# Kernel optimization log

Hardware: AMD Instinct MI355X
Metric: run time of the kernel (lower is better)

The kernel has to match this reference:

```python
import jax, jax.numpy as jnp
import numpy as np

NUM_HEADS = 10
NEG_BIG = -2.0**32 + 1.0  # padding value used before softmax in the original
MASK_ADDER = -10000.0     # additive directional mask value


def setup_inputs() -> dict:
    key = jax.random.key(0)
    k1, k2, k3, k4, k5 = jax.random.split(key, 5)
    B, T, D, U = 8, 1024, 640, 640
    x = jax.random.normal(k1, (B, T, D), dtype=jnp.float32)
    mask = jax.random.randint(k2, (B, T), 0, 2, dtype=jnp.int32)
    s = 1.0 / np.sqrt(D)
    Wq = jax.random.normal(k3, (D, U), dtype=jnp.float32) * s
    Wk = jax.random.normal(k4, (D, U), dtype=jnp.float32) * s
    Wv = jax.random.normal(k5, (D, U), dtype=jnp.float32) * s
    return {"x": x, "mask": mask, "Wq": Wq, "Wk": Wk, "Wv": Wv}


def reference(x, mask, Wq, Wk, Wv):
    B, T, _ = x.shape
    H = NUM_HEADS
    U = Wq.shape[1]
    d = U // H

    # projections (no bias)
    Q = x @ Wq  # [B,T,U]
    K = x @ Wk
    V = x @ Wv

    # tf split(axis=2)+concat(axis=0) == head-major layout [H,B,T,d]
    def to_heads(t):
        return t.reshape(B, T, H, d).transpose(2, 0, 1, 3)

    Qh, Kh, Vh = to_heads(Q), to_heads(K), to_heads(V)

    scores = jnp.einsum('hbqd,hbkd->hbqk', Qh, Kh) / jnp.sqrt(jnp.float32(d))

    # key padding mask: sign(sum|K|) per key position
    key_m = jnp.sign(jnp.sum(jnp.abs(Kh), axis=-1))  # [H,B,T]
    scores = jnp.where(key_m[:, :, None, :] == 0, jnp.float32(NEG_BIG), scores)

    # directional mask: 'forward' -> attend strictly to past (row > col)
    row = jnp.arange(T)[:, None]
    col = jnp.arange(T)[None, :]
    allowed = (row > col).astype(scores.dtype)  # [T,T]
    scores = scores + (1.0 - allowed) * MASK_ADDER

    attn = jax.nn.softmax(scores, axis=-1)

    # post-softmax multiplicative query mask
    query_m = jnp.sign(jnp.sum(jnp.abs(Qh), axis=-1))  # [H,B,T]
    attn = attn * query_m[:, :, :, None]

    out = jnp.einsum('hbqk,hbkd->hbqd', attn, Vh)  # [H,B,T,d]
    out = out.transpose(1, 2, 0, 3).reshape(B, T, U)  # concat heads back on feature dim

    out = out * mask[:, :, None].astype(jnp.float32)
    return out
```

## Files before the change

### kernel.cpp

```cpp
#include <hip/hip_runtime.h>
#include <hip/hip_bf16.h>
#include <stdint.h>

#define B_DIM 8
#define T_DIM 1024
#define D_DIM 640
#define H_DIM 10
#define LOG2E 1.442695041f

typedef unsigned short ushort_t;
typedef __attribute__((ext_vector_type(8))) short short8;
typedef __attribute__((ext_vector_type(4))) float f32x4;
typedef __attribute__((ext_vector_type(16))) float f32x16;
typedef __attribute__((ext_vector_type(4))) unsigned int u32x4;

__device__ __forceinline__ ushort_t f32_to_bf16(float f) {
    unsigned int u = __builtin_bit_cast(unsigned int, f);
    u += 0x7fffu + ((u >> 16) & 1u);
    return (ushort_t)(u >> 16);
}
__device__ __forceinline__ float v_exp2(float x) {
    float r; asm("v_exp_f32 %0, %1" : "=v"(r) : "v"(x)); return r;
}
__device__ __forceinline__ unsigned cvt_pk_bf16(float a, float b) {
    unsigned r; asm("v_cvt_pk_bf16_f32 %0, %1, %2" : "=v"(r) : "v"(a), "v"(b)); return r;
}
__device__ __forceinline__ void gload16(const void* g, void* l) {
    auto gp = reinterpret_cast<const __attribute__((address_space(1))) uint32_t*>(
        reinterpret_cast<uintptr_t>(g));
    auto lp = reinterpret_cast<__attribute__((address_space(3))) uint32_t*>(
        reinterpret_cast<uintptr_t>(l));
    __builtin_amdgcn_global_load_lds(gp, lp, 16, 0, 0);
}

__constant__ int SPERM[32] = {0,31,30,29,28,27,26,25,24,23,22,21,20,19,18,17,
                              16,15,14,13,12,11,10,9,8,7,6,5,4,3,2,1};

__global__ __launch_bounds__(256) void convwt(
    const float* __restrict__ x,
    const float* __restrict__ Wq, const float* __restrict__ Wk, const float* __restrict__ Wv,
    ushort_t* __restrict__ xb, ushort_t* __restrict__ Wt)
{
    const int tid = threadIdx.x;
    if (blockIdx.x < 300) {
        const int w = blockIdx.x / 100, rem = blockIdx.x % 100;
        const int k0 = (rem % 10) * 64, n0 = (rem / 10) * 64;
        const float* W = (w == 0) ? Wq : (w == 1) ? Wk : Wv;
        ushort_t* Wo = Wt + (size_t)w * D_DIM * D_DIM;

        __shared__ alignas(16) ushort_t st[64][72];
        const int r = tid >> 2, cs = (tid & 3) * 16;
        #pragma unroll
        for (int j = 0; j < 4; ++j) {
            float4 v = *reinterpret_cast<const float4*>(
                &W[(size_t)(k0 + r) * D_DIM + n0 + cs + j * 4]);
            st[r][cs + j * 4 + 0] = f32_to_bf16(v.x);
            st[r][cs + j * 4 + 1] = f32_to_bf16(v.y);
            st[r][cs + j * 4 + 2] = f32_to_bf16(v.z);
            st[r][cs + j * 4 + 3] = f32_to_bf16(v.w);
        }
        __syncthreads();
        const int nr = tid >> 2, ks = (tid & 3) * 16;
        ushort_t tmp[16];
        #pragma unroll
        for (int j = 0; j < 16; ++j) tmp[j] = st[ks + j][nr];
        ushort_t* dst = &Wo[(size_t)(n0 + nr) * D_DIM + k0 + ks];
        *reinterpret_cast<short8*>(dst)     = *reinterpret_cast<const short8*>(&tmp[0]);
        *reinterpret_cast<short8*>(dst + 8) = *reinterpret_cast<const short8*>(&tmp[8]);
    } else {
        const int n8 = (B_DIM * T_DIM * D_DIM) / 8;
        for (int i = (blockIdx.x - 300) * 256 + tid; i < n8; i += 2048 * 256) {
            float4 a = *reinterpret_cast<const float4*>(&x[i * 8]);
            float4 b = *reinterpret_cast<const float4*>(&x[i * 8 + 4]);
            ushort_t o[8] = {f32_to_bf16(a.x), f32_to_bf16(a.y), f32_to_bf16(a.z), f32_to_bf16(a.w),
                             f32_to_bf16(b.x), f32_to_bf16(b.y), f32_to_bf16(b.z), f32_to_bf16(b.w)};
            *reinterpret_cast<short8*>(&xb[i * 8]) = *reinterpret_cast<const short8*>(o);
        }
    }
}

__global__ __launch_bounds__(256) void gemm_qkv(
    const ushort_t* __restrict__ xb, const ushort_t* __restrict__ Wt,
    const int* __restrict__ msk,
    ushort_t* __restrict__ QF, ushort_t* __restrict__ KF, ushort_t* __restrict__ VF,
    float* __restrict__ qs, ushort_t* __restrict__ km16)
{
    const int L = blockIdx.x;
    const int xcd = L & 7, j = L >> 3;
    const int m0 = (xcd * 8 + (j & 7)) * 128;
    const int nz = j >> 3;
    const int n0 = (nz % 5) * 128;
    const int w  = nz / 5;

    const ushort_t* Wm = Wt + (size_t)w * D_DIM * D_DIM;

    __shared__ alignas(16) ushort_t As[128 * 64];
    __shared__ alignas(16) ushort_t Bs[128 * 64];

    const int tid = threadIdx.x;
    const int lane = tid & 63, wave = tid >> 6;
    const int lo = lane & 15, g = lane >> 4;
    const int wm = wave >> 1, wn = wave & 1;
    const int srow = tid >> 3, schunk = tid & 7;

    f32x4 acc[4][4];
    #pragma unroll
    for (int i = 0; i < 4; ++i)
        #pragma unroll
        for (int jj = 0; jj < 4; ++jj) acc[i][jj] = (f32x4){0.f, 0.f, 0.f, 0.f};

    for (int k0 = 0; k0 < D_DIM; k0 += 64) {
        #pragma unroll
        for (int i = 0; i < 4; ++i) {
            int row = i * 32 + srow;
            int sc = schunk ^ (row & 7);
            gload16(&xb[(size_t)(m0 + row) * D_DIM + k0 + sc * 8], &As[i * 2048 + tid * 8]);
            gload16(&Wm[(size_t)(n0 + row) * D_DIM + k0 + sc * 8], &Bs[i * 2048 + tid * 8]);
        }
        __syncthreads();
        #pragma unroll
        for (int ks = 0; ks < 2; ++ks) {
            short8 af[4], bf[4];
            #pragma unroll
            for (int t = 0; t < 4; ++t) {
                int arow = wm * 64 + t * 16 + lo;
                int ach = (ks * 4 + g) ^ (arow & 7);
                af[t] = *reinterpret_cast<const short8*>(&As[arow * 64 + ach * 8]);
                int brow = wn * 64 + t * 16 + lo;
                int bch = (ks * 4 + g) ^ (brow & 7);
                bf[t] = *reinterpret_cast<const short8*>(&Bs[brow * 64 + bch * 8]);
            }
            __builtin_amdgcn_s_setprio(1);
            #pragma unroll
            for (int mi = 0; mi < 4; ++mi)
                #pragma unroll
                for (int ni = 0; ni < 4; ++ni)
                    acc[mi][ni] = __builtin_amdgcn_mfma_f32_16x16x32_bf16(
                        af[mi], bf[ni], acc[mi][ni], 0, 0, 0);
            __builtin_amdgcn_s_setprio(0);
        }
        __syncthreads();
    }

    const int hh = (n0 >> 6) + wn;
    const int bb = m0 >> 10;
    const int hb = hh * 8 + bb;
    const int ktw = ((m0 & 1023) >> 6) + wm;

    if (w == 2) {
        const int hiv = g >> 1, jj0 = (g & 1) * 4;
        #pragma unroll
        for (int mi = 0; mi < 4; ++mi)
            #pragma unroll
            for (int ni = 0; ni < 4; ++ni) {
                const int df = ni >> 1, l31v = (ni & 1) * 16 + lo;
                size_t idx = ((((size_t)(hb * 16 + ktw) * 4 + mi) * 2 + df) * 64
                              + hiv * 32 + l31v) * 8 + jj0;
                ushort4 o = make_ushort4(f32_to_bf16(acc[mi][ni][0]), f32_to_bf16(acc[mi][ni][1]),
                                         f32_to_bf16(acc[mi][ni][2]), f32_to_bf16(acc[mi][ni][3]));
                *reinterpret_cast<ushort4*>(&VF[idx]) = o;
            }
    } else {
        #pragma unroll
        for (int mi = 0; mi < 4; ++mi)
            #pragma unroll
            for (int r = 0; r < 4; ++r) {
                float s_ = fabsf(acc[mi][0][r]) + fabsf(acc[mi][1][r])
                         + fabsf(acc[mi][2][r]) + fabsf(acc[mi][3][r]);
                #pragma unroll
                for (int m = 1; m < 16; m <<= 1) s_ += __shfl_xor(s_, m);
                if (lo == 0) {
                    int row = m0 + wm * 64 + mi * 16 + g * 4 + r;
                    int rowid = hh * 8192 + row;
                    if (w == 0) qs[rowid] = (s_ > 0.f ? 1.f : 0.f) * (float)msk[row];
                    else        km16[rowid] = (s_ > 0.f) ? (ushort_t)0x3F80 : (ushort_t)0;
                }
            }
        const int hi2 = lo >> 3, jjq = lo & 7;
        const int s32base = ((m0 & 1023) + wm * 64) >> 5;
        #pragma unroll
        for (int mi = 0; mi < 4; ++mi)
            #pragma unroll
            for (int ni = 0; ni < 4; ++ni)
                #pragma unroll
                for (int r = 0; r < 4; ++r) {
                    int l31 = (mi & 1) * 16 + g * 4 + r;
                    if (w == 0) {
                        int s32 = s32base + (mi >> 1);
                        size_t idx = (((size_t)(hb * 32 + s32) * 4 + ni) * 64
                                      + hi2 * 32 + l31) * 8 + jjq;
                        QF[idx] = f32_to_bf16(acc[mi][ni][r]);
                    } else {
                        int f = (mi >> 1) & 1;
                        size_t idx = ((((size_t)(hb * 16 + ktw) * 2 + f) * 4 + ni) * 64
                                      + hi2 * 32 + l31) * 8 + jjq;
                        KF[idx] = f32_to_bf16(acc[mi][ni][r]);
                    }
                }
    }
}

#define LOADK(KB_, KT_IDX) do {                                                  \
    const ushort_t* KT_ = &KFh[(KT_IDX) * 4096];                                 \
    _Pragma("unroll")                                                            \
    for (int f_ = 0; f_ < 2; ++f_)                                               \
        _Pragma("unroll")                                                        \
        for (int kc_ = 0; kc_ < 4; ++kc_)                                        \
            KB_[f_][kc_] = *reinterpret_cast<const short8*>(                     \
                &KT_[(f_ * 4 + kc_) * 512 + lane * 8]);                          \
} while (0)

#define COMPUTE_TILE(KBUF, KT_IDX) do {                                          \
    const int k0_ = (KT_IDX) * 64;                                               \
    const ushort_t* VT_ = &VFh[(size_t)(KT_IDX) * 4096];                         \
    short8 vfA_[2][2], vfB_[2][2];                                               \
    _Pragma("unroll")                                                            \
    for (int c_ = 0; c_ < 2; ++c_)                                               \
        _Pragma("unroll")                                                        \
        for (int df_ = 0; df_ < 2; ++df_)                                        \
            vfA_[c_][df_] = *reinterpret_cast<const short8*>(                    \
                &VT_[(c_ * 2 + df_) * 512 + lane * 8]);                          \
    ushort4 kq_[2][4];                                                           \
    _Pragma("unroll")                                                            \
    for (int f_ = 0; f_ < 2; ++f_)                                               \
        _Pragma("unroll")                                                        \
        for (int rr_ = 0; rr_ < 4; ++rr_)                                        \
            kq_[f_][rr_] = *reinterpret_cast<const ushort4*>(                    \
                &kmr[k0_ + f_ * 32 + rr_ * 8 + hi * 4]);                         \
    unsigned pk_[2][8];                                                          \
    _Pragma("unroll")                                                            \
    for (int f_ = 0; f_ < 2; ++f_) {                                             \
        f32x16 sf_;                                                              \
        _Pragma("unroll")                                                        \
        for (int i_ = 0; i_ < 16; ++i_) sf_[i_] = 0.f;                           \
        __builtin_amdgcn_s_setprio(1);                                           \
        _Pragma("unroll")                                                        \
        for (int kc_ = 0; kc_ < 4; ++kc_)                                        \
            sf_ = __builtin_amdgcn_mfma_f32_32x32x16_bf16(KBUF[f_][kc_],         \
                                                          qf[kc_], sf_, 0, 0, 0);\
        __builtin_amdgcn_s_setprio(0);                                           \
        if (f_ == 0) {                                                           \
            _Pragma("unroll")                                                    \
            for (int c_ = 0; c_ < 2; ++c_)                                       \
                _Pragma("unroll")                                                \
                for (int df_ = 0; df_ < 2; ++df_)                                \
                    vfB_[c_][df_] = *reinterpret_cast<const short8*>(            \
                        &VT_[((c_ + 2) * 2 + df_) * 512 + lane * 8]);            \
        }                                                                        \
        _Pragma("unroll")                                                        \
        for (int rr_ = 0; rr_ < 4; ++rr_) {                                      \
            const int kbase_ = k0_ + f_ * 32 + rr_ * 8 + hi * 4;                 \
            const ushort_t* kmv_ =                                               \
                reinterpret_cast<const ushort_t*>(&kq_[f_][rr_]);                \
            float p_[4];                                                         \
            _Pragma("unroll")                                                    \
            for (int ri_ = 0; ri_ < 4; ++ri_) {                                  \
                float cc_ = (kbase_ + ri_ >= trow) ? cB : cA;                    \
                cc_ = kmv_[ri_] ? cc_ : -1e30f;                                  \
                p_[ri_] = v_exp2(fmaf(sf_[rr_ * 4 + ri_], S2, cc_));             \
                lacc += p_[ri_];                                                 \
            }                                                                    \
            pk_[f_][rr_ * 2 + 0] = cvt_pk_bf16(p_[0], p_[1]);                    \
            pk_[f_][rr_ * 2 + 1] = cvt_pk_bf16(p_[2], p_[3]);                    \
        }                                                                        \
    }                                                                            \
    _Pragma("unroll")                                                            \
    for (int c_ = 0; c_ < 4; ++c_) {                                             \
        const int f_ = c_ >> 1, o_ = (c_ & 1) * 4;                               \
        unsigned a0_ = pk_[f_][o_ + 0], b0_ = pk_[f_][o_ + 2];                   \
        unsigned a1_ = pk_[f_][o_ + 1], b1_ = pk_[f_][o_ + 3];                   \
        if (v1) {                                                                \
            asm volatile("v_permlane32_swap_b32 %0, %1" : "+v"(b0_), "+v"(a0_)); \
            asm volatile("v_permlane32_swap_b32 %0, %1" : "+v"(b1_), "+v"(a1_)); \
        } else {                                                                 \
            asm volatile("v_permlane32_swap_b32 %0, %1" : "+v"(a0_), "+v"(b0_)); \
            asm volatile("v_permlane32_swap_b32 %0, %1" : "+v"(a1_), "+v"(b1_)); \
        }                                                                        \
        u32x4 pau_ = {a0_, a1_, b0_, b1_};                                       \
        short8 pa_ = __builtin_bit_cast(short8, pau_);                           \
        short8 v0_ = (c_ < 2) ? vfA_[c_][0] : vfB_[c_ - 2][0];                   \
        short8 v1f_ = (c_ < 2) ? vfA_[c_][1] : vfB_[c_ - 2][1];                  \
        __builtin_amdgcn_s_setprio(1);                                           \
        of0 = __builtin_amdgcn_mfma_f32_32x32x16_bf16(pa_, v0_, of0, 0, 0, 0);   \
        of1 = __builtin_amdgcn_mfma_f32_32x32x16_bf16(pa_, v1f_, of1, 0, 0, 0);  \
        __builtin_amdgcn_s_setprio(0);                                           \
    }                                                                            \
} while (0)

__global__ __launch_bounds__(256, 2) void attn_wave(
    const ushort_t* __restrict__ QF, const ushort_t* __restrict__ KF,
    const ushort_t* __restrict__ VF, const float* __restrict__ qs,
    const ushort_t* __restrict__ km16, float* __restrict__ out)
{
    __shared__ float scs[4][32];
    const int tid = threadIdx.x, lane = tid & 63, wave = tid >> 6;
    const int l31 = lane & 31, hi = lane >> 5;

    const int bid = blockIdx.x, xcd = bid & 7, j = bid >> 3;
    const int g8 = xcd + 8 * (j % 10), qg = j / 10;
    const int s = SPERM[qg * 4 + wave], q0 = s * 32;
    const int b = g8 & 7, h = g8 >> 3, hb = h * 8 + b;

    unsigned pva = (unsigned)lane, pvb = 64u + (unsigned)lane;
    asm volatile("v_permlane32_swap_b32 %0, %1" : "+v"(pva), "+v"(pvb));
    const bool v1 = (__builtin_amdgcn_readfirstlane((int)pva) >= 96);

    const ushort_t* QFh = QF + (size_t)(hb * 32 + s) * 2048;
    const ushort_t* KFh = KF + (size_t)hb * 16 * 4096;
    const ushort_t* VFh = VF + (size_t)hb * 16 * 4096;
    const ushort_t* kmr = km16 + (size_t)hb * 1024;

    short8 qf[4];
    #pragma unroll
    for (int kc = 0; kc < 4; ++kc)
        qf[kc] = *reinterpret_cast<const short8*>(&QFh[kc * 512 + lane * 8]);

    bool anyPrior = false;
    for (int c = 0; c < (q0 >> 6); ++c) {
        ushort_t v = kmr[c * 64 + lane];
        anyPrior = anyPrior || (__ballot(v != 0) != 0ull);
    }
    float M;
    {
        ushort_t v = kmr[(q0 & ~63) + lane];
        unsigned long long bal = __ballot(v != 0);
        unsigned long long pre = bal & ((1ull << ((q0 & 63) + l31)) - 1ull);
        M = (anyPrior || pre != 0ull) ? 16.f : -9984.f;
    }
    const float cA = -M * LOG2E;
    const float cB = cA - 10000.0f * LOG2E;
    const float S2 = 0.125f * LOG2E;
    const int trow = q0 + l31;

    float lacc = 0.f;
    f32x16 of0, of1;
    #pragma unroll
    for (int i = 0; i < 16; ++i) { of0[i] = 0.f; of1[i] = 0.f; }

    const int ktend = (s == 0) ? 16 : ((s >> 1) + 1);

    short8 kA[2][4], kB[2][4];
    LOADK(kA, 0);
    int kt = 0;
    for (; kt + 2 <= ktend; kt += 2) {
        LOADK(kB, kt + 1);
        COMPUTE_TILE(kA, kt);
        if (kt + 2 < ktend) LOADK(kA, kt + 2);
        COMPUTE_TILE(kB, kt + 1);
    }
    if (kt < ktend) COMPUTE_TILE(kA, kt);

    float ltot = lacc + __shfl_xor(lacc, 32);
    if (hi == 0)
        scs[wave][l31] = qs[(size_t)hb * 1024 + q0 + l31] / ltot;
    const size_t obase = ((size_t)b * T_DIM + q0) * D_DIM + h * 64;
    #pragma unroll
    for (int reg = 0; reg < 16; ++reg) {
        const int qrow = (reg & 3) + 8 * (reg >> 2) + 4 * hi;
        const float sc = scs[wave][qrow];
        out[obase + (size_t)qrow * D_DIM + l31]      = of0[reg] * sc;
        out[obase + (size_t)qrow * D_DIM + 32 + l31] = of1[reg] * sc;
    }
}

extern "C" void kernel_launch(void* const* d_in, const int* in_sizes, int n_in,
                              void* d_out, int out_size, void* d_ws, size_t ws_size,
                              hipStream_t stream)
{
    const float* x   = (const float*)d_in[0];
    const int*   msk = (const int*)d_in[1];
    const float* Wq  = (const float*)d_in[2];
    const float* Wk  = (const float*)d_in[3];
    const float* Wv  = (const float*)d_in[4];
    float* out = (float*)d_out;

    char* ws = (char*)d_ws;
    ushort_t* xb = (ushort_t*)(ws);
    ushort_t* Wt = (ushort_t*)(ws + 10485760);
    ushort_t* QF = (ushort_t*)(ws + 12943360);
    ushort_t* KF = (ushort_t*)(ws + 23429120);
    ushort_t* VF = (ushort_t*)(ws + 33914880);
    float*    qs = (float*)(ws + 44400640);
    ushort_t* km = (ushort_t*)(ws + 44728320);
    if (ws_size < 44892160) return;

    convwt<<<2348, 256, 0, stream>>>(x, Wq, Wk, Wv, xb, Wt);
    gemm_qkv<<<960, 256, 0, stream>>>(xb, Wt, msk, QF, KF, VF, qs, km);
    attn_wave<<<640, 256, 0, stream>>>(QF, KF, VF, qs, km, out);
}
```

Baseline: 79.84 us.

## Split each query strip's key tiles across four waves and merge via LDS

The attention kernel previously gave each wave its own 32-row query strip and walked all key tiles serially, with double-buffered K loads. Now a block of four waves shares a single query strip. Each wave handles every fourth key tile, and wave 0 sums the partial outputs and row sums from LDS before normalizing and storing. This gives 4x more blocks, raises launch bounds to 3, and drops the software K prefetch. The aim is to shorten the long causal strips that dominate runtime. The cost is extra LDS traffic, a block-level barrier, idle waves on short strips, and redundant Q loads and mask prologue work per wave.

```diff
diff --git a/kernel.cpp b/kernel.cpp
--- a/kernel.cpp
+++ b/kernel.cpp
@@ -200,19 +200,17 @@
     }
 }
 
-#define LOADK(KB_, KT_IDX) do {                                                  \
-    const ushort_t* KT_ = &KFh[(KT_IDX) * 4096];                                 \
+#define DO_TILE(KT_IDX) do {                                                     \
+    const int k0_ = (KT_IDX) * 64;                                               \
+    const ushort_t* KT_ = &KFh[(size_t)(KT_IDX) * 4096];                         \
+    const ushort_t* VT_ = &VFh[(size_t)(KT_IDX) * 4096];                         \
+    short8 kA_[2][4];                                                            \
     _Pragma("unroll")                                                            \
     for (int f_ = 0; f_ < 2; ++f_)                                               \
         _Pragma("unroll")                                                        \
         for (int kc_ = 0; kc_ < 4; ++kc_)                                        \
-            KB_[f_][kc_] = *reinterpret_cast<const short8*>(                     \
+            kA_[f_][kc_] = *reinterpret_cast<const short8*>(                     \
                 &KT_[(f_ * 4 + kc_) * 512 + lane * 8]);                          \
-} while (0)
-
-#define COMPUTE_TILE(KBUF, KT_IDX) do {                                          \
-    const int k0_ = (KT_IDX) * 64;                                               \
-    const ushort_t* VT_ = &VFh[(size_t)(KT_IDX) * 4096];                         \
     short8 vfA_[2][2], vfB_[2][2];                                               \
     _Pragma("unroll")                                                            \
     for (int c_ = 0; c_ < 2; ++c_)                                               \
@@ -236,7 +234,7 @@
         __builtin_amdgcn_s_setprio(1);                                           \
         _Pragma("unroll")                                                        \
         for (int kc_ = 0; kc_ < 4; ++kc_)                                        \
-            sf_ = __builtin_amdgcn_mfma_f32_32x32x16_bf16(KBUF[f_][kc_],         \
+            sf_ = __builtin_amdgcn_mfma_f32_32x32x16_bf16(kA_[f_][kc_],          \
                                                           qf[kc_], sf_, 0, 0, 0);\
         __builtin_amdgcn_s_setprio(0);                                           \
         if (f_ == 0) {                                                           \
@@ -287,18 +285,21 @@
     }                                                                            \
 } while (0)
 
-__global__ __launch_bounds__(256, 2) void attn_wave(
+__global__ __launch_bounds__(256, 3) void attn_strip(
     const ushort_t* __restrict__ QF, const ushort_t* __restrict__ KF,
     const ushort_t* __restrict__ VF, const float* __restrict__ qs,
     const ushort_t* __restrict__ km16, float* __restrict__ out)
 {
-    __shared__ float scs[4][32];
+    __shared__ alignas(16) float mrg[3 * 64 * 36];
+
     const int tid = threadIdx.x, lane = tid & 63, wave = tid >> 6;
     const int l31 = lane & 31, hi = lane >> 5;
 
-    const int bid = blockIdx.x, xcd = bid & 7, j = bid >> 3;
-    const int g8 = xcd + 8 * (j % 10), qg = j / 10;
-    const int s = SPERM[qg * 4 + wave], q0 = s * 32;
+    const int bid = blockIdx.x;
+    const int xcd = bid & 7, i = bid >> 3;
+    const int sr = i / 10, grp = i % 10;
+    const int g8 = xcd + 8 * grp;
+    const int s = SPERM[sr], q0 = s * 32;
     const int b = g8 & 7, h = g8 >> 3, hb = h * 8 + b;
 
     unsigned pva = (unsigned)lane, pvb = 64u + (unsigned)lane;
@@ -335,31 +336,50 @@
     float lacc = 0.f;
     f32x16 of0, of1;
     #pragma unroll
-    for (int i = 0; i < 16; ++i) { of0[i] = 0.f; of1[i] = 0.f; }
+    for (int i2 = 0; i2 < 16; ++i2) { of0[i2] = 0.f; of1[i2] = 0.f; }
 
     const int ktend = (s == 0) ? 16 : ((s >> 1) + 1);
 
-    short8 kA[2][4], kB[2][4];
-    LOADK(kA, 0);
-    int kt = 0;
-    for (; kt + 2 <= ktend; kt += 2) {
-        LOADK(kB, kt + 1);
-        COMPUTE_TILE(kA, kt);
-        if (kt + 2 < ktend) LOADK(kA, kt + 2);
-        COMPUTE_TILE(kB, kt + 1);
-    }
-    if (kt < ktend) COMPUTE_TILE(kA, kt);
-
-    float ltot = lacc + __shfl_xor(lacc, 32);
-    if (hi == 0)
-        scs[wave][l31] = qs[(size_t)hb * 1024 + q0 + l31] / ltot;
-    const size_t obase = ((size_t)b * T_DIM + q0) * D_DIM + h * 64;
-    #pragma unroll
-    for (int reg = 0; reg < 16; ++reg) {
-        const int qrow = (reg & 3) + 8 * (reg >> 2) + 4 * hi;
-        const float sc = scs[wave][qrow];
-        out[obase + (size_t)qrow * D_DIM + l31]      = of0[reg] * sc;
-        out[obase + (size_t)qrow * D_DIM + 32 + l31] = of1[reg] * sc;
+    for (int kt = wave; kt < ktend; kt += 4)
+        DO_TILE(kt);
+
+    if (wave != 0) {
+        float* dst = &mrg[((wave - 1) * 64 + lane) * 36];
+        #pragma unroll
+        for (int q = 0; q < 4; ++q) {
+            reinterpret_cast<float4*>(dst)[q] =
+                make_float4(of0[q * 4 + 0], of0[q * 4 + 1], of0[q * 4 + 2], of0[q * 4 + 3]);
+            reinterpret_cast<float4*>(dst)[4 + q] =
+                make_float4(of1[q * 4 + 0], of1[q * 4 + 1], of1[q * 4 + 2], of1[q * 4 + 3]);
+        }
+        dst[32] = lacc;
+    }
+    __syncthreads();
+    if (wave == 0) {
+        #pragma unroll
+        for (int w2 = 0; w2 < 3; ++w2) {
+            const float* src = &mrg[(w2 * 64 + lane) * 36];
+            #pragma unroll
+            for (int q = 0; q < 4; ++q) {
+                float4 t0 = reinterpret_cast<const float4*>(src)[q];
+                of0[q * 4 + 0] += t0.x; of0[q * 4 + 1] += t0.y;
+                of0[q * 4 + 2] += t0.z; of0[q * 4 + 3] += t0.w;
+                float4 t1 = reinterpret_cast<const float4*>(src)[4 + q];
+                of1[q * 4 + 0] += t1.x; of1[q * 4 + 1] += t1.y;
+                of1[q * 4 + 2] += t1.z; of1[q * 4 + 3] += t1.w;
+            }
+            lacc += src[32];
+        }
+        float ltot = lacc + __shfl_xor(lacc, 32);
+        float scale = qs[(size_t)hb * 1024 + q0 + l31] / ltot;
+        const size_t obase = ((size_t)b * T_DIM + q0) * D_DIM + h * 64;
+        #pragma unroll
+        for (int reg = 0; reg < 16; ++reg) {
+            const int qrow = (reg & 3) + 8 * (reg >> 2) + 4 * hi;
+            const float sc = __shfl(scale, qrow);
+            out[obase + (size_t)qrow * D_DIM + l31]      = of0[reg] * sc;
+            out[obase + (size_t)qrow * D_DIM + 32 + l31] = of1[reg] * sc;
+        }
     }
 }
 
@@ -386,5 +406,5 @@
 
     convwt<<<2348, 256, 0, stream>>>(x, Wq, Wk, Wv, xb, Wt);
     gemm_qkv<<<960, 256, 0, stream>>>(xb, Wt, msk, QF, KF, VF, qs, km);
-    attn_wave<<<640, 256, 0, stream>>>(QF, KF, VF, qs, km, out);
-}
+    attn_strip<<<2560, 256, 0, stream>>>(QF, KF, VF, qs, km, out);
+}
```

Result: no change. 79.18 us (-0.8%).
